# Performance work log

Measured on AMD Instinct MI355X. Metric: run time of the kernel, lower is better.

Reference implementation:

```python
import jax, jax.numpy as jnp
import numpy as np

# NSA hyperparameters (HFNSACore defaults)
KS, ST, BS = 32, 16, 64            # kernel_size, stride, block_size
TOP_N, NINIT, NLOCAL, WIN = 16, 2, 1, 512
NEG = -1e30
BIG = 1e30


def setup_inputs() -> dict:
    key = jax.random.key(0)
    k1, k2, k3, k4 = jax.random.split(key, 4)
    T, Hq, Hkv, D = 2048, 16, 1, 128
    q = jax.random.normal(k1, (T, Hq, D), jnp.float32)
    k = jax.random.normal(k2, (T, Hkv, D), jnp.float32)
    v = jax.random.normal(k3, (T, Hkv, D), jnp.float32)
    combine_weight = jax.random.normal(k4, (T, Hq, 3), jnp.float32)
    cu_seqlens = jnp.array([0, T], dtype=jnp.int32)  # single varlen sequence
    return {"q": q, "k": k, "v": v, "combine_weight": combine_weight, "cu_seqlens": cu_seqlens}


def _nsa_forward(q, k, v, cw):
    T, Hq, Dqk = q.shape
    Hkv = k.shape[1]
    G = Hq // Hkv                      # GQA group size
    Dv = v.shape[-1]
    scale = Dqk ** -0.5
    M = (T - KS) // ST + 1             # number of compressed kv tokens
    NB = (T + BS - 1) // BS            # number of selection blocks
    t_pos = jnp.arange(T)

    # ---- CompressKV (version='mean'): mean-pool sliding blocks of size KS, stride ST ----
    blk_idx = jnp.arange(M)[:, None] * ST + jnp.arange(KS)[None, :]   # [M, KS]
    cmp_k = k[blk_idx].mean(axis=1)    # [M, Hkv, Dqk]
    cmp_v = v[blk_idx].mean(axis=1)    # [M, Hkv, Dv]

    qg = q.reshape(T, Hkv, G, Dqk)

    # ---- compress_attn: causal attention over compressed kv ----
    # query t can see cmp token j only if its block is fully in the past: j*ST + KS <= t+1
    cmp_scores = jnp.einsum('tkgd,mkd->tkgm', qg, cmp_k) * scale      # [T,Hkv,G,M]
    cmp_valid = (jnp.arange(M)[None, :] * ST + KS) <= (t_pos[:, None] + 1)  # [T,M]
    cmp_scores = jnp.where(cmp_valid[:, None, None, :], cmp_scores, NEG)
    p_cmp = jax.nn.softmax(cmp_scores, axis=-1)
    p_cmp = jnp.where(cmp_valid.any(-1)[:, None, None, None], p_cmp, 0.0)
    cmp_o = jnp.einsum('tkgm,mkd->tkgd', p_cmp, cmp_v).reshape(T, Hq, Dv)

    # ---- slc_topk_indices: map cmp probs to selection-block scores (scale_slc_p) ----
    ju, bu = KS // ST, BS // ST        # extents in stride units
    j = np.arange(M)[:, None]
    b = np.arange(NB)[None, :]
    ov = np.maximum(0, np.minimum(j + ju, (b + 1) * bu) - np.maximum(j, b * bu))
    Wmap = jnp.asarray(ov / ju, jnp.float32)                          # [M, NB] overlap fraction
    slc_p = jnp.einsum('tkgm,mb->tkb', p_cmp, Wmap)                   # sum probs over group heads
    cur_blk = t_pos // BS
    bidx = jnp.arange(NB)
    future = bidx[None, :] > cur_blk[:, None]                         # [T,NB]
    forced = (bidx[None, :] < NINIT) | ((bidx[None, :] <= cur_blk[:, None]) & (bidx[None, :] > cur_blk[:, None] - NLOCAL))
    slc_p = jnp.where(future[:, None, :], NEG, slc_p)
    slc_p = jnp.where(forced[:, None, :], BIG, slc_p)
    topk = jax.lax.top_k(slc_p, TOP_N)[1]                             # [T,Hkv,TOP_N]

    causal = t_pos[:, None] >= t_pos[None, :]                         # [T,T]

    # ---- select_attn: causal attention restricted to selected blocks ----
    key_blk = t_pos // BS
    sel = (topk[..., None] == key_blk[None, None, None, :]).any(axis=2)  # [T,Hkv,T]
    smask = sel & causal[:, None, :]
    slc_scores = jnp.einsum('tkgd,skd->tkgs', qg, k) * scale
    slc_scores = jnp.where(smask[:, :, None, :], slc_scores, NEG)
    slc_o = jnp.einsum('tkgs,skd->tkgd', jax.nn.softmax(slc_scores, axis=-1), v).reshape(T, Hq, Dv)

    # ---- swa_varlen_func: sliding-window causal attention ----
    wmask = causal & ((t_pos[:, None] - t_pos[None, :]) < WIN)
    swa_scores = jnp.einsum('tkgd,skd->tkgs', qg, k) * scale
    swa_scores = jnp.where(wmask[None, None, :, :].transpose(2, 0, 1, 3)[:, :, 0:1, :].squeeze(2)[:, None, None, :] if False else wmask[:, None, None, :], swa_scores, NEG)
    swa_o = jnp.einsum('tkgs,skd->tkgd', jax.nn.softmax(swa_scores, axis=-1), v).reshape(T, Hq, Dv)

    # ---- fused_sigmoid_combine ----
    w = jax.nn.sigmoid(cw)                                            # [T,Hq,3]
    return w[..., 0:1] * cmp_o + w[..., 1:2] * slc_o + w[..., 2:3] * swa_o


def reference(q, k, v, combine_weight, cu_seqlens):
    # single-sequence varlen: cu_seqlens = [0, T]
    return _nsa_forward(q, k, v, combine_weight)
```

## Files before the change

### kernel.cpp

```cpp
#include <hip/hip_runtime.h>
#include <math.h>

constexpr int kT    = 2048;
constexpr int kHQ   = 16;
constexpr int kD    = 128;
constexpr int kKS   = 32;
constexpr int kST   = 16;
constexpr int kBS   = 64;
constexpr int kM    = (kT - kKS) / kST + 1;
constexpr int kNB   = (kT + kBS - 1) / kBS;
constexpr int kTopN = 16;
constexpr int kNInit = 2;
constexpr int kWIN  = 512;
constexpr float kNEG = -1e30f;
constexpr float kScale = 0.08838834764831845f;
constexpr float kScaleL2 = kScale * 1.4426950408889634f;

constexpr int kPSt = 72;
constexpr int kPL  = 136;

constexpr int kOxS0 = 0;
constexpr int kPS0  = 4096;
constexpr int kOxS1 = 6400;
constexpr int kPS1  = 10496;
constexpr int kOxW1 = 10496;
constexpr int kMl1  = 14592;
constexpr int kUreg = 15104;

typedef __attribute__((ext_vector_type(8))) short short8;
typedef __attribute__((ext_vector_type(4))) short short4v;
typedef __attribute__((ext_vector_type(8))) _Float16 half8;
typedef __attribute__((ext_vector_type(4))) _Float16 half4v;
typedef __attribute__((ext_vector_type(4))) float floatx4;

__device__ inline short f2bf(float x) {
    unsigned u = __float_as_uint(x);
    unsigned r = (u + 0x7fffu + ((u >> 16) & 1u)) >> 16;
    return (short)r;
}
__device__ inline float b2f(short h) {
    return __uint_as_float(((unsigned)(unsigned short)h) << 16);
}

__global__ __launch_bounds__(256) void k_stage(
        const float* __restrict__ k, const float* __restrict__ v,
        short* __restrict__ kb2, _Float16* __restrict__ vt2,
        short* __restrict__ ck2h, short* __restrict__ ck2l,
        short* __restrict__ cv2) {
    const int bid = blockIdx.x;
    const int tid = threadIdx.x;
    __shared__ _Float16 vls[64 * 132];

    if (bid < 32) {
        const int b = bid;
        #pragma unroll
        for (int p = 0; p < 4; ++p) {
            const int idx = p * 256 + tid;
            const int g = idx >> 6;
            const int lane2 = idx & 63;
            const int kt = g >> 2, c = g & 3;
            const int l15v = lane2 & 15, quadv = lane2 >> 4;
            const float* src = k + (size_t)(b * 64 + kt * 16 + l15v) * kD + c * 32 + quadv * 8;
            const float4 f0 = *(const float4*)(src);
            const float4 f1 = *(const float4*)(src + 4);
            short8 s;
            s[0] = f2bf(f0.x); s[1] = f2bf(f0.y); s[2] = f2bf(f0.z); s[3] = f2bf(f0.w);
            s[4] = f2bf(f1.x); s[5] = f2bf(f1.y); s[6] = f2bf(f1.z); s[7] = f2bf(f1.w);
            *(short8*)(kb2 + ((size_t)b * 1024 + idx) * 8) = s;
        }
    } else if (bid < 64) {
        const int b = bid - 32;
        #pragma unroll
        for (int p = 0; p < 8; ++p) {
            const int idx = p * 256 + tid;
            const int r = idx >> 5;
            const int d4 = (idx & 31) * 4;
            const float4 f = *(const float4*)(v + (size_t)(b * 64 + r) * kD + d4);
            _Float16* dst = &vls[r * 132 + d4];
            dst[0] = (_Float16)f.x; dst[1] = (_Float16)f.y;
            dst[2] = (_Float16)f.z; dst[3] = (_Float16)f.w;
        }
        __syncthreads();
        #pragma unroll
        for (int p = 0; p < 4; ++p) {
            const int idx = p * 256 + tid;
            const int g = idx >> 6;
            const int lane2 = idx & 63;
            const int n8 = g >> 1, kc = g & 1;
            const int l15v = lane2 & 15, quadv = lane2 >> 4;
            half8 h;
            #pragma unroll
            for (int j = 0; j < 8; ++j) {
                const int col = kc * 32 + quadv * 8 + j;
                const int w = (col & 3) * 16 + (col >> 2);
                h[j] = vls[w * 132 + n8 * 16 + l15v];
            }
            *(half8*)(vt2 + ((size_t)b * 1024 + idx) * 8) = h;
        }
    } else {
        const int m = (bid - 64) * 2 + (tid >> 7);
        const int d = tid & 127;
        float sk = 0.f, sv = 0.f;
        if (m < kM) {
            const int base = m * kST;
            #pragma unroll
            for (int i = 0; i < kKS; ++i) {
                sk += k[(size_t)(base + i) * kD + d];
                sv += v[(size_t)(base + i) * kD + d];
            }
            sk *= (1.0f / kKS);
            sv *= (1.0f / kKS);
        }
        const short hi = f2bf(sk);
        const short lo = f2bf(sk - b2f(hi));
        const int mt = m >> 4, l15m = m & 15;
        const int c = d >> 5, quadv = (d >> 3) & 3, j = d & 7;
        const int kdst = ((mt * 4 + c) * 64 + quadv * 16 + l15m) * 8 + j;
        ck2h[kdst] = hi;
        ck2l[kdst] = lo;
        const int nt = d >> 4, l15d = d & 15;
        const int pc = (m & 64) + 4 * (m & 15) + ((m & 63) >> 4);
        const int cp = pc >> 5, quadp = (pc >> 3) & 3, jp = pc & 7;
        cv2[((nt * 4 + cp) * 64 + quadp * 16 + l15d) * 8 + jp] = f2bf(sv);
    }
}

__global__ __launch_bounds__(128, 4) void k_nsa(
        const float* __restrict__ q, const float* __restrict__ cw,
        const short* __restrict__ ck2h, const short* __restrict__ ck2l,
        const short* __restrict__ cv2, const short* __restrict__ kb2,
        const _Float16* __restrict__ vt2, float* __restrict__ out) {
    const int tid = threadIdx.x;
    const int wave = tid >> 6;
    const int lane = tid & 63;
    const int l15 = lane & 15;
    const int quad = lane >> 4;
    const int t = kT - 1 - blockIdx.x;

    __shared__ float sp[kNB];
    __shared__ unsigned selm_s;
    __shared__ short ocst[64 * 32];
    __shared__ __align__(16) char ureg[kUreg];

    _Float16* const PSme = (_Float16*)(ureg + (wave ? kPS1 : kPS0));
    short* const oxMine  = (short*)(ureg + (wave ? kOxS1 : kOxS0));

    short8 qh[4];
    {
        const float* qp = q + ((size_t)t * kHQ + l15) * kD + quad * 8;
        #pragma unroll
        for (int c = 0; c < 4; ++c) {
            const float4 f0 = *(const float4*)(qp + c * 32);
            const float4 f1 = *(const float4*)(qp + c * 32 + 4);
            const float xs[8] = {f0.x, f0.y, f0.z, f0.w, f1.x, f1.y, f1.z, f1.w};
            #pragma unroll
            for (int j = 0; j < 8; ++j) qh[c][j] = f2bf(xs[j] * kScaleL2);
        }
    }

    const int nvalid = (t >= kKS - 1) ? min(kM, (t - (kKS - 1)) / kST + 1) : 0;
    const int cur = t >> 6;

    if (wave == 0) {
        short8 ql[4];
        {
            const float* qp = q + ((size_t)t * kHQ + l15) * kD + quad * 8;
            #pragma unroll
            for (int c = 0; c < 4; ++c) {
                const float4 f0 = *(const float4*)(qp + c * 32);
                const float4 f1 = *(const float4*)(qp + c * 32 + 4);
                const float xs[8] = {f0.x, f0.y, f0.z, f0.w, f1.x, f1.y, f1.z, f1.w};
                #pragma unroll
                for (int j = 0; j < 8; ++j)
                    ql[c][j] = f2bf(xs[j] * kScaleL2 - b2f(qh[c][j]));
            }
        }
        short* const p_lds = (short*)ureg;
        floatx4 sacc[8];
        #pragma unroll
        for (int mt = 0; mt < 8; ++mt) {
            sacc[mt] = (floatx4){0, 0, 0, 0};
            #pragma unroll
            for (int c = 0; c < 4; ++c) {
                const short8 Ah = *(const short8*)(ck2h + ((mt * 4 + c) * 64 + lane) * 8);
                const short8 Al = *(const short8*)(ck2l + ((mt * 4 + c) * 64 + lane) * 8);
                sacc[mt] = __builtin_amdgcn_mfma_f32_16x16x32_bf16(Ah, qh[c], sacc[mt], 0, 0, 0);
                sacc[mt] = __builtin_amdgcn_mfma_f32_16x16x32_bf16(Ah, ql[c], sacc[mt], 0, 0, 0);
                sacc[mt] = __builtin_amdgcn_mfma_f32_16x16x32_bf16(Al, qh[c], sacc[mt], 0, 0, 0);
            }
        }
        float mx = kNEG;
        #pragma unroll
        for (int mt = 0; mt < 8; ++mt)
            #pragma unroll
            for (int r = 0; r < 4; ++r) {
                const int m = mt * 16 + quad * 4 + r;
                const float s = (m < nvalid) ? sacc[mt][r] : kNEG;
                sacc[mt][r] = s;
                mx = fmaxf(mx, s);
            }
        mx = fmaxf(mx, __shfl_xor(mx, 16));
        mx = fmaxf(mx, __shfl_xor(mx, 32));
        float sum = 0.f;
        #pragma unroll
        for (int mt = 0; mt < 8; ++mt)
            #pragma unroll
            for (int r = 0; r < 4; ++r) {
                const int m = mt * 16 + quad * 4 + r;
                const float ev = (m < nvalid) ? exp2f(sacc[mt][r] - mx) : 0.f;
                sacc[mt][r] = ev;
                sum += ev;
            }
        sum += __shfl_xor(sum, 16);
        sum += __shfl_xor(sum, 32);
        const float inv = (nvalid > 0) ? (1.f / sum) : 0.f;

        float Z[8], Y[8];
        #pragma unroll
        for (int mt = 0; mt < 8; ++mt) {
            const float p0 = sacc[mt][0] * inv, p1 = sacc[mt][1] * inv;
            const float p2 = sacc[mt][2] * inv, p3 = sacc[mt][3] * inv;
            sacc[mt][0] = p0; sacc[mt][1] = p1; sacc[mt][2] = p2; sacc[mt][3] = p3;
            Z[mt] = p0 + p1 + p2 + 0.5f * p3;
            Y[mt] = p3;
        }
        #pragma unroll
        for (int g = 0; g < 2; ++g)
            #pragma unroll
            for (int r = 0; r < 4; ++r) {
                short4v s4;
                s4[0] = f2bf(sacc[4 * g + 0][r]); s4[1] = f2bf(sacc[4 * g + 1][r]);
                s4[2] = f2bf(sacc[4 * g + 2][r]); s4[3] = f2bf(sacc[4 * g + 3][r]);
                *(short4v*)&p_lds[l15 * kPL + g * 64 + 16 * quad + 4 * r] = s4;
            }
        #pragma unroll
        for (int mt = 0; mt < 8; ++mt) {
            #pragma unroll
            for (int o = 1; o <= 8; o <<= 1) {
                Z[mt] += __shfl_xor(Z[mt], o, 16);
                Y[mt] += __shfl_xor(Y[mt], o, 16);
            }
        }
        const int srcl = ((quad + 3) & 3) * 16 + l15;
        #pragma unroll
        for (int mt = 0; mt < 8; ++mt) {
            const float up  = __shfl(Y[mt], srcl);
            const float upm = __shfl(Y[(mt + 7) & 7], srcl);
            const float pv = quad ? up : (mt ? upm : 0.f);
            const int b = 4 * mt + quad;
            float x = Z[mt] + 0.5f * pv;
            if (b > cur) x = kNEG;
            if (b < kNInit || b == cur) x = 1e30f;
            if (l15 == 0) sp[b] = x;
        }
        bool selp = false;
        if (lane < kNB) {
            const float xv = sp[lane];
            int rank = 0;
            #pragma unroll
            for (int b2 = 0; b2 < kNB; ++b2) {
                const float y = sp[b2];
                rank += (y > xv || (y == xv && b2 < lane)) ? 1 : 0;
            }
            selp = rank < kTopN;
        }
        const unsigned sm = (unsigned)__ballot(selp);
        if (lane == 0) selm_s = sm;

        short8 ap[4];
        #pragma unroll
        for (int c = 0; c < 4; ++c)
            ap[c] = *(const short8*)&p_lds[l15 * kPL + c * 32 + quad * 8];
        #pragma unroll
        for (int nt = 0; nt < 8; ++nt) {
            floatx4 oc = (floatx4){0, 0, 0, 0};
            #pragma unroll
            for (int c = 0; c < 4; ++c) {
                const short8 bv = *(const short8*)(cv2 + ((nt * 4 + c) * 64 + lane) * 8);
                oc = __builtin_amdgcn_mfma_f32_16x16x32_bf16(ap[c], bv, oc, 0, 0, 0);
            }
            short4v s4;
            s4[0] = f2bf(oc[0]); s4[1] = f2bf(oc[1]);
            s4[2] = f2bf(oc[2]); s4[3] = f2bf(oc[3]);
            *(short4v*)&ocst[lane * 32 + nt * 4] = s4;
        }
    }
    __syncthreads();

    const unsigned selm = selm_s;
    const int lob = max(0, (t - (kWIN - 1)) >> 6);
    const unsigned lm = 0xFFFFFFFFu >> (31 - cur);

    float mS = kNEG, lS = 0.f;
    float mW = kNEG, lW = 0.f;

    {
        floatx4 osel[8];
        #pragma unroll
        for (int n8 = 0; n8 < 8; ++n8) osel[n8] = (floatx4){0, 0, 0, 0};

        unsigned a = selm & lm;
        int bi = 0;
        while (a) {
            const int b = __builtin_ctz(a);
            a &= a - 1u;
            const bool mine = ((bi & 1) != wave);
            ++bi;
            if (!mine) continue;

            const short* kbb = kb2 + ((size_t)b * 1024 + lane) * 8;
            floatx4 acc[4];
            {
                short8 kreg[2][4];
                #pragma unroll
                for (int kt = 0; kt < 2; ++kt)
                    #pragma unroll
                    for (int c = 0; c < 4; ++c)
                        kreg[kt][c] = *(const short8*)(kbb + (kt * 4 + c) * 512);
                #pragma unroll
                for (int kt = 0; kt < 2; ++kt) {
                    acc[kt] = (floatx4){0, 0, 0, 0};
                    #pragma unroll
                    for (int c = 0; c < 4; ++c)
                        acc[kt] = __builtin_amdgcn_mfma_f32_16x16x32_bf16(kreg[kt][c], qh[c], acc[kt], 0, 0, 0);
                }
                #pragma unroll
                for (int kt = 0; kt < 2; ++kt)
                    #pragma unroll
                    for (int c = 0; c < 4; ++c)
                        kreg[kt][c] = *(const short8*)(kbb + ((kt + 2) * 4 + c) * 512);
                #pragma unroll
                for (int kt = 0; kt < 2; ++kt) {
                    acc[kt + 2] = (floatx4){0, 0, 0, 0};
                    #pragma unroll
                    for (int c = 0; c < 4; ++c)
                        acc[kt + 2] = __builtin_amdgcn_mfma_f32_16x16x32_bf16(kreg[kt][c], qh[c], acc[kt + 2], 0, 0, 0);
                }
            }

            const int kbo = b * kBS + quad * 4;
            float bm = kNEG;
            #pragma unroll
            for (int kt = 0; kt < 4; ++kt)
                #pragma unroll
                for (int r = 0; r < 4; ++r) {
                    const int key = kbo + kt * 16 + r;
                    if (key <= t) bm = fmaxf(bm, acc[kt][r]);
                }
            bm = fmaxf(bm, __shfl_xor(bm, 16));
            bm = fmaxf(bm, __shfl_xor(bm, 32));
            const float mn = fmaxf(mS, bm);
            const float al = exp2f(mS - mn);

            float sum = 0.f;
            #pragma unroll
            for (int r = 0; r < 4; ++r) {
                half4v hs;
                #pragma unroll
                for (int kt = 0; kt < 4; ++kt) {
                    const int key = kbo + kt * 16 + r;
                    const float e0 = (key <= t) ? exp2f(acc[kt][r] - mn) : 0.f;
                    sum += e0;
                    hs[kt] = (_Float16)e0;
                }
                *(half4v*)&PSme[l15 * kPSt + 16 * quad + 4 * r] = hs;
            }
            sum += __shfl_xor(sum, 16);
            sum += __shfl_xor(sum, 32);
            lS = lS * al + sum; mS = mn;

            float alh[4];
            #pragma unroll
            for (int r = 0; r < 4; ++r) alh[r] = __shfl(al, quad * 4 + r);
            const half8 ap0 = *(const half8*)&PSme[l15 * kPSt + quad * 8];
            const half8 ap1 = *(const half8*)&PSme[l15 * kPSt + 32 + quad * 8];
            const _Float16* vtb = vt2 + ((size_t)b * 1024 + lane) * 8;
            {
                half8 vr[4][2];
                #pragma unroll
                for (int n8 = 0; n8 < 4; ++n8) {
                    vr[n8][0] = *(const half8*)(vtb + (n8 * 2 + 0) * 512);
                    vr[n8][1] = *(const half8*)(vtb + (n8 * 2 + 1) * 512);
                }
                #pragma unroll
                for (int n8 = 0; n8 < 4; ++n8) {
                    #pragma unroll
                    for (int r = 0; r < 4; ++r) osel[n8][r] *= alh[r];
                    osel[n8] = __builtin_amdgcn_mfma_f32_16x16x32_f16(ap0, vr[n8][0], osel[n8], 0, 0, 0);
                    osel[n8] = __builtin_amdgcn_mfma_f32_16x16x32_f16(ap1, vr[n8][1], osel[n8], 0, 0, 0);
                }
                #pragma unroll
                for (int n8 = 0; n8 < 4; ++n8) {
                    vr[n8][0] = *(const half8*)(vtb + ((n8 + 4) * 2 + 0) * 512);
                    vr[n8][1] = *(const half8*)(vtb + ((n8 + 4) * 2 + 1) * 512);
                }
                #pragma unroll
                for (int n8 = 0; n8 < 4; ++n8) {
                    #pragma unroll
                    for (int r = 0; r < 4; ++r) osel[n8 + 4][r] *= alh[r];
                    osel[n8 + 4] = __builtin_amdgcn_mfma_f32_16x16x32_f16(ap0, vr[n8][0], osel[n8 + 4], 0, 0, 0);
                    osel[n8 + 4] = __builtin_amdgcn_mfma_f32_16x16x32_f16(ap1, vr[n8][1], osel[n8 + 4], 0, 0, 0);
                }
            }
        }

        #pragma unroll
        for (int n8 = 0; n8 < 8; ++n8) {
            short4v s4;
            #pragma unroll
            for (int r = 0; r < 4; ++r) s4[r] = f2bf(osel[n8][r]);
            *(short4v*)&oxMine[lane * 32 + n8 * 4] = s4;
        }
    }

    floatx4 oswa[8];
    #pragma unroll
    for (int n8 = 0; n8 < 8; ++n8) oswa[n8] = (floatx4){0, 0, 0, 0};
    {
        unsigned a = lm & ~((1u << lob) - 1u);
        int bi = 0;
        while (a) {
            const int b = __builtin_ctz(a);
            a &= a - 1u;
            const bool mine = ((bi & 1) != wave);
            ++bi;
            if (!mine) continue;

            const short* kbb = kb2 + ((size_t)b * 1024 + lane) * 8;
            floatx4 acc[4];
            {
                short8 kreg[2][4];
                #pragma unroll
                for (int kt = 0; kt < 2; ++kt)
                    #pragma unroll
                    for (int c = 0; c < 4; ++c)
                        kreg[kt][c] = *(const short8*)(kbb + (kt * 4 + c) * 512);
                #pragma unroll
                for (int kt = 0; kt < 2; ++kt) {
                    acc[kt] = (floatx4){0, 0, 0, 0};
                    #pragma unroll
                    for (int c = 0; c < 4; ++c)
                        acc[kt] = __builtin_amdgcn_mfma_f32_16x16x32_bf16(kreg[kt][c], qh[c], acc[kt], 0, 0, 0);
                }
                #pragma unroll
                for (int kt = 0; kt < 2; ++kt)
                    #pragma unroll
                    for (int c = 0; c < 4; ++c)
                        kreg[kt][c] = *(const short8*)(kbb + ((kt + 2) * 4 + c) * 512);
                #pragma unroll
                for (int kt = 0; kt < 2; ++kt) {
                    acc[kt + 2] = (floatx4){0, 0, 0, 0};
                    #pragma unroll
                    for (int c = 0; c < 4; ++c)
                        acc[kt + 2] = __builtin_amdgcn_mfma_f32_16x16x32_bf16(kreg[kt][c], qh[c], acc[kt + 2], 0, 0, 0);
                }
            }

            const int kbo = b * kBS + quad * 4;
            float bm = kNEG;
            #pragma unroll
            for (int kt = 0; kt < 4; ++kt)
                #pragma unroll
                for (int r = 0; r < 4; ++r) {
                    const int key = kbo + kt * 16 + r;
                    if (key <= t && (t - key) < kWIN) bm = fmaxf(bm, acc[kt][r]);
                }
            bm = fmaxf(bm, __shfl_xor(bm, 16));
            bm = fmaxf(bm, __shfl_xor(bm, 32));
            const float mn = fmaxf(mW, bm);
            const float al = exp2f(mW - mn);

            float sum = 0.f;
            #pragma unroll
            for (int r = 0; r < 4; ++r) {
                half4v hw;
                #pragma unroll
                for (int kt = 0; kt < 4; ++kt) {
                    const int key = kbo + kt * 16 + r;
                    const float e0 = (key <= t && (t - key) < kWIN) ? exp2f(acc[kt][r] - mn) : 0.f;
                    sum += e0;
                    hw[kt] = (_Float16)e0;
                }
                *(half4v*)&PSme[l15 * kPSt + 16 * quad + 4 * r] = hw;
            }
            sum += __shfl_xor(sum, 16);
            sum += __shfl_xor(sum, 32);
            lW = lW * al + sum; mW = mn;

            float alh[4];
            #pragma unroll
            for (int r = 0; r < 4; ++r) alh[r] = __shfl(al, quad * 4 + r);
            const half8 ap0 = *(const half8*)&PSme[l15 * kPSt + quad * 8];
            const half8 ap1 = *(const half8*)&PSme[l15 * kPSt + 32 + quad * 8];
            const _Float16* vtb = vt2 + ((size_t)b * 1024 + lane) * 8;
            {
                half8 vr[4][2];
                #pragma unroll
                for (int n8 = 0; n8 < 4; ++n8) {
                    vr[n8][0] = *(const half8*)(vtb + (n8 * 2 + 0) * 512);
                    vr[n8][1] = *(const half8*)(vtb + (n8 * 2 + 1) * 512);
                }
                #pragma unroll
                for (int n8 = 0; n8 < 4; ++n8) {
                    #pragma unroll
                    for (int r = 0; r < 4; ++r) oswa[n8][r] *= alh[r];
                    oswa[n8] = __builtin_amdgcn_mfma_f32_16x16x32_f16(ap0, vr[n8][0], oswa[n8], 0, 0, 0);
                    oswa[n8] = __builtin_amdgcn_mfma_f32_16x16x32_f16(ap1, vr[n8][1], oswa[n8], 0, 0, 0);
                }
                #pragma unroll
                for (int n8 = 0; n8 < 4; ++n8) {
                    vr[n8][0] = *(const half8*)(vtb + ((n8 + 4) * 2 + 0) * 512);
                    vr[n8][1] = *(const half8*)(vtb + ((n8 + 4) * 2 + 1) * 512);
                }
                #pragma unroll
                for (int n8 = 0; n8 < 4; ++n8) {
                    #pragma unroll
                    for (int r = 0; r < 4; ++r) oswa[n8 + 4][r] *= alh[r];
                    oswa[n8 + 4] = __builtin_amdgcn_mfma_f32_16x16x32_f16(ap0, vr[n8][0], oswa[n8 + 4], 0, 0, 0);
                    oswa[n8 + 4] = __builtin_amdgcn_mfma_f32_16x16x32_f16(ap1, vr[n8][1], oswa[n8 + 4], 0, 0, 0);
                }
            }
        }
    }

    if (wave == 1) {
        short* const oxW = (short*)(ureg + kOxW1);
        #pragma unroll
        for (int n8 = 0; n8 < 8; ++n8) {
            short4v w4;
            #pragma unroll
            for (int r = 0; r < 4; ++r) w4[r] = f2bf(oswa[n8][r]);
            *(short4v*)&oxW[lane * 32 + n8 * 4] = w4;
        }
        if (quad == 0)
            *(float4*)&((float*)(ureg + kMl1))[l15 * 4] = make_float4(mS, lS, mW, lW);
    }
    __syncthreads();

    if (wave == 0) {
        const short* const oxS0 = (const short*)(ureg + kOxS0);
        const short* const oxS1 = (const short*)(ureg + kOxS1);
        const short* const oxW1 = (const short*)(ureg + kOxW1);
        const float* const ml1  = (const float*)(ureg + kMl1);

        #pragma unroll
        for (int r = 0; r < 4; ++r) {
            const int h = quad * 4 + r;
            const float m0S = __shfl(mS, h), l0S = __shfl(lS, h);
            const float m0W = __shfl(mW, h), l0W = __shfl(lW, h);
            const float4 a1 = *(const float4*)&ml1[h * 4];
            const float mMS = fmaxf(m0S, a1.x);
            const float c0S = exp2f(m0S - mMS);
            const float c1S = exp2f(a1.x - mMS);
            const float liS = 1.f / (l0S * c0S + a1.y * c1S);
            const float mMW = fmaxf(m0W, a1.z);
            const float c0W = exp2f(m0W - mMW);
            const float c1W = exp2f(a1.z - mMW);
            const float liW = 1.f / (l0W * c0W + a1.w * c1W);
            const float cwa = cw[((size_t)t * kHQ + h) * 3 + 0];
            const float cwb = cw[((size_t)t * kHQ + h) * 3 + 1];
            const float cwc = cw[((size_t)t * kHQ + h) * 3 + 2];
            const float w0 = 1.f / (1.f + __expf(-cwa));
            const float w1 = 1.f / (1.f + __expf(-cwb));
            const float w2 = 1.f / (1.f + __expf(-cwc));
            float* op = out + ((size_t)t * kHQ + h) * kD + l15;
            #pragma unroll
            for (int n8 = 0; n8 < 8; ++n8) {
                const int j = n8 * 4 + r;
                const float sM = (b2f(oxS0[lane * 32 + j]) * c0S + b2f(oxS1[lane * 32 + j]) * c1S) * liS;
                const float wM = (oswa[n8][r] * c0W + b2f(oxW1[lane * 32 + j]) * c1W) * liW;
                const float oc = b2f(ocst[lane * 32 + j]);
                op[n8 * 16] = w0 * oc + w1 * sM + w2 * wM;
            }
        }
    }
}

extern "C" void kernel_launch(void* const* d_in, const int* in_sizes, int n_in,
                              void* d_out, int out_size, void* d_ws, size_t ws_size,
                              hipStream_t stream) {
    const float* q  = (const float*)d_in[0];
    const float* k  = (const float*)d_in[1];
    const float* v  = (const float*)d_in[2];
    const float* cw = (const float*)d_in[3];
    float* out = (float*)d_out;

    short* kb2    = (short*)d_ws;
    _Float16* vt2 = (_Float16*)(kb2 + 32 * 1024 * 8);
    short* ck2h   = (short*)(vt2 + 32 * 1024 * 8);
    short* ck2l   = ck2h + 32 * 64 * 8;
    short* cv2    = ck2l + 32 * 64 * 8;

    k_stage<<<dim3(128), dim3(256), 0, stream>>>(k, v, kb2, vt2, ck2h, ck2l, cv2);
    k_nsa<<<dim3(kT), dim3(128), 0, stream>>>(q, cw, ck2h, ck2l, cv2, kb2, vt2, out);
}
```

Baseline: 152.8 us.

## Accumulate branch outputs into global memory to shrink LDS and raise occupancy

The compressed, selected and sliding-window branch outputs are now written or added straight into the output buffer in stages. Previously all partial results were staged in LDS and combined once at the end. This lets one shared dump buffer be reused, cutting shared memory from about 19KB to under 9KB, and the launch bound is raised to allow 8 blocks per CU. The cost is extra global read-modify-write traffic on the output and an added barrier between stages.

```diff
diff --git a/kernel.cpp b/kernel.cpp
--- a/kernel.cpp
+++ b/kernel.cpp
@@ -19,13 +19,11 @@
 constexpr int kPSt = 72;
 constexpr int kPL  = 136;
 
-constexpr int kOxS0 = 0;
-constexpr int kPS0  = 4096;
-constexpr int kOxS1 = 6400;
-constexpr int kPS1  = 10496;
-constexpr int kOxW1 = 10496;
-constexpr int kMl1  = 14592;
-constexpr int kUreg = 15104;
+constexpr int kPS0 = 0;
+constexpr int kPS1 = 2304;
+constexpr int kDmp = 4608;
+constexpr int kMl  = 8704;
+constexpr int kShm = 8832;
 
 typedef __attribute__((ext_vector_type(8))) short short8;
 typedef __attribute__((ext_vector_type(4))) short short4v;
@@ -125,7 +123,7 @@
     }
 }
 
-__global__ __launch_bounds__(128, 4) void k_nsa(
+__global__ __launch_bounds__(128, 8) void k_nsa(
         const float* __restrict__ q, const float* __restrict__ cw,
         const short* __restrict__ ck2h, const short* __restrict__ ck2l,
         const short* __restrict__ cv2, const short* __restrict__ kb2,
@@ -139,11 +137,9 @@
 
     __shared__ float sp[kNB];
     __shared__ unsigned selm_s;
-    __shared__ short ocst[64 * 32];
-    __shared__ __align__(16) char ureg[kUreg];
-
-    _Float16* const PSme = (_Float16*)(ureg + (wave ? kPS1 : kPS0));
-    short* const oxMine  = (short*)(ureg + (wave ? kOxS1 : kOxS0));
+    __shared__ __align__(16) char shm[kShm];
+
+    _Float16* const PSme = (_Float16*)(shm + (wave ? kPS1 : kPS0));
 
     short8 qh[4];
     {
@@ -175,7 +171,7 @@
                     ql[c][j] = f2bf(xs[j] * kScaleL2 - b2f(qh[c][j]));
             }
         }
-        short* const p_lds = (short*)ureg;
+        short* const p_lds = (short*)shm;
         floatx4 sacc[8];
         #pragma unroll
         for (int mt = 0; mt < 8; ++mt) {
@@ -271,6 +267,13 @@
         #pragma unroll
         for (int c = 0; c < 4; ++c)
             ap[c] = *(const short8*)&p_lds[l15 * kPL + c * 32 + quad * 8];
+        float w0h[4];
+        #pragma unroll
+        for (int r = 0; r < 4; ++r) {
+            const int h = quad * 4 + r;
+            const float cwa = cw[((size_t)t * kHQ + h) * 3 + 0];
+            w0h[r] = 1.f / (1.f + __expf(-cwa));
+        }
         #pragma unroll
         for (int nt = 0; nt < 8; ++nt) {
             floatx4 oc = (floatx4){0, 0, 0, 0};
@@ -279,10 +282,11 @@
                 const short8 bv = *(const short8*)(cv2 + ((nt * 4 + c) * 64 + lane) * 8);
                 oc = __builtin_amdgcn_mfma_f32_16x16x32_bf16(ap[c], bv, oc, 0, 0, 0);
             }
-            short4v s4;
-            s4[0] = f2bf(oc[0]); s4[1] = f2bf(oc[1]);
-            s4[2] = f2bf(oc[2]); s4[3] = f2bf(oc[3]);
-            *(short4v*)&ocst[lane * 32 + nt * 4] = s4;
+            #pragma unroll
+            for (int r = 0; r < 4; ++r) {
+                const int h = quad * 4 + r;
+                out[((size_t)t * kHQ + h) * kD + nt * 16 + l15] = w0h[r] * oc[r];
+            }
         }
     }
     __syncthreads();
@@ -291,10 +295,8 @@
     const int lob = max(0, (t - (kWIN - 1)) >> 6);
     const unsigned lm = 0xFFFFFFFFu >> (31 - cur);
 
-    float mS = kNEG, lS = 0.f;
-    float mW = kNEG, lW = 0.f;
-
     {
+        float mS = kNEG, lS = 0.f;
         floatx4 osel[8];
         #pragma unroll
         for (int n8 = 0; n8 < 8; ++n8) osel[n8] = (floatx4){0, 0, 0, 0};
@@ -404,15 +406,43 @@
             }
         }
 
-        #pragma unroll
-        for (int n8 = 0; n8 < 8; ++n8) {
-            short4v s4;
-            #pragma unroll
-            for (int r = 0; r < 4; ++r) s4[r] = f2bf(osel[n8][r]);
-            *(short4v*)&oxMine[lane * 32 + n8 * 4] = s4;
+        if (wave == 1) {
+            short* const dmp = (short*)(shm + kDmp);
+            #pragma unroll
+            for (int n8 = 0; n8 < 8; ++n8) {
+                short4v s4;
+                #pragma unroll
+                for (int r = 0; r < 4; ++r) s4[r] = f2bf(osel[n8][r]);
+                *(short4v*)&dmp[lane * 32 + n8 * 4] = s4;
+            }
+            if (quad == 0) ((float2*)(shm + kMl))[l15] = make_float2(mS, lS);
+        }
+        __syncthreads();
+        if (wave == 0) {
+            const short* const ox1 = (const short*)(shm + kDmp);
+            const float2* const ml1 = (const float2*)(shm + kMl);
+            #pragma unroll
+            for (int r = 0; r < 4; ++r) {
+                const int h = quad * 4 + r;
+                const float m0 = __shfl(mS, h), l0 = __shfl(lS, h);
+                const float2 s1 = ml1[h];
+                const float mM = fmaxf(m0, s1.x);
+                const float c0 = exp2f(m0 - mM);
+                const float c1 = exp2f(s1.x - mM);
+                const float li = 1.f / (l0 * c0 + s1.y * c1);
+                const float cwb = cw[((size_t)t * kHQ + h) * 3 + 1];
+                const float w1 = 1.f / (1.f + __expf(-cwb));
+                float* op = out + ((size_t)t * kHQ + h) * kD + l15;
+                #pragma unroll
+                for (int n8 = 0; n8 < 8; ++n8) {
+                    const float sM = (osel[n8][r] * c0 + b2f(ox1[lane * 32 + n8 * 4 + r]) * c1) * li;
+                    op[n8 * 16] += w1 * sM;
+                }
+            }
         }
     }
 
+    float mW = kNEG, lW = 0.f;
     floatx4 oswa[8];
     #pragma unroll
     for (int n8 = 0; n8 < 8; ++n8) oswa[n8] = (floatx4){0, 0, 0, 0};
@@ -523,54 +553,38 @@
         }
     }
 
+    __syncthreads();
     if (wave == 1) {
-        short* const oxW = (short*)(ureg + kOxW1);
+        short* const dmp = (short*)(shm + kDmp);
         #pragma unroll
         for (int n8 = 0; n8 < 8; ++n8) {
             short4v w4;
             #pragma unroll
             for (int r = 0; r < 4; ++r) w4[r] = f2bf(oswa[n8][r]);
-            *(short4v*)&oxW[lane * 32 + n8 * 4] = w4;
-        }
-        if (quad == 0)
-            *(float4*)&((float*)(ureg + kMl1))[l15 * 4] = make_float4(mS, lS, mW, lW);
+            *(short4v*)&dmp[lane * 32 + n8 * 4] = w4;
+        }
+        if (quad == 0) ((float2*)(shm + kMl))[l15] = make_float2(mW, lW);
     }
     __syncthreads();
-
     if (wave == 0) {
-        const short* const oxS0 = (const short*)(ureg + kOxS0);
-        const short* const oxS1 = (const short*)(ureg + kOxS1);
-        const short* const oxW1 = (const short*)(ureg + kOxW1);
-        const float* const ml1  = (const float*)(ureg + kMl1);
-
+        const short* const ox1 = (const short*)(shm + kDmp);
+        const float2* const ml1 = (const float2*)(shm + kMl);
         #pragma unroll
         for (int r = 0; r < 4; ++r) {
             const int h = quad * 4 + r;
-            const float m0S = __shfl(mS, h), l0S = __shfl(lS, h);
-            const float m0W = __shfl(mW, h), l0W = __shfl(lW, h);
-            const float4 a1 = *(const float4*)&ml1[h * 4];
-            const float mMS = fmaxf(m0S, a1.x);
-            const float c0S = exp2f(m0S - mMS);
-            const float c1S = exp2f(a1.x - mMS);
-            const float liS = 1.f / (l0S * c0S + a1.y * c1S);
-            const float mMW = fmaxf(m0W, a1.z);
-            const float c0W = exp2f(m0W - mMW);
-            const float c1W = exp2f(a1.z - mMW);
-            const float liW = 1.f / (l0W * c0W + a1.w * c1W);
-            const float cwa = cw[((size_t)t * kHQ + h) * 3 + 0];
-            const float cwb = cw[((size_t)t * kHQ + h) * 3 + 1];
+            const float m0 = __shfl(mW, h), l0 = __shfl(lW, h);
+            const float2 s1 = ml1[h];
+            const float mM = fmaxf(m0, s1.x);
+            const float c0 = exp2f(m0 - mM);
+            const float c1 = exp2f(s1.x - mM);
+            const float li = 1.f / (l0 * c0 + s1.y * c1);
             const float cwc = cw[((size_t)t * kHQ + h) * 3 + 2];
-            const float w0 = 1.f / (1.f + __expf(-cwa));
-            const float w1 = 1.f / (1.f + __expf(-cwb));
             const float w2 = 1.f / (1.f + __expf(-cwc));
             float* op = out + ((size_t)t * kHQ + h) * kD + l15;
             #pragma unroll
             for (int n8 = 0; n8 < 8; ++n8) {
-                const int j = n8 * 4 + r;
-                const float sM = (b2f(oxS0[lane * 32 + j]) * c0S + b2f(oxS1[lane * 32 + j]) * c1S) * liS;
-                const float wM = (oswa[n8][r] * c0W + b2f(oxW1[lane * 32 + j]) * c1W) * liW;
-                const float oc = b2f(ocst[lane * 32 + j]);
-                op[n8 * 16] = w0 * oc + w1 * sM + w2 * wM;
+                const float wM = (oswa[n8][r] * c0 + b2f(ox1[lane * 32 + n8 * 4 + r]) * c1) * li;
+                op[n8 * 16] += w2 * wM;
             }
         }
     }
```

Measured after the change: 385.6 us. 152% more time.
